# Kernel optimization log

Hardware: AMD Instinct MI355X
Metric: run time of the kernel (lower is better)

The kernel has to match this reference:

```python
import jax, jax.numpy as jnp
import numpy as np

N, E, F, H, S, L, B = 20000, 320000, 64, 256, 32, 128, 16
TAU = 1.0
EPS = 1e-9


def _glorot(k, i, o):
    return (jax.random.normal(k, (i, o), jnp.float32) / np.sqrt(i)).astype(jnp.float32)


def _mlp3(h, w1, b1, w2, b2, w3, b3):
    h = jax.nn.relu(h @ w1 + b1)
    h = jax.nn.relu(h @ w2 + b2)
    return h @ w3 + b3


def _gnn_layer(x, src, dst, w1, b1, w2, b2, w3, b3):
    # PyG: x_i = x[dst] (target), x_j = x[src] (source); aggregate 'add' at target
    m = _mlp3(jnp.concatenate([x[dst], x[src]], axis=1), w1, b1, w2, b2, w3, b3)  # [E, H]
    return jax.ops.segment_sum(m, dst, num_segments=N)  # [N, H]


def _layer_norm(x, g, b):
    mu = x.mean(-1, keepdims=True)
    var = ((x - mu) ** 2).mean(-1, keepdims=True)
    return (x - mu) * jax.lax.rsqrt(var + 1e-5) * g + b


def setup_inputs() -> dict:
    key = jax.random.key(0)
    ks = jax.random.split(key, 32)
    d = {
        'x': jax.random.normal(ks[0], (N, F), jnp.float32),
        'u': jax.random.uniform(ks[1], (N, S), jnp.float32, minval=1e-6, maxval=1.0 - 1e-6),
        'edge_index': jax.random.randint(ks[2], (2, E), 0, N, jnp.int32),
        'batch': jnp.sort(jax.random.randint(ks[3], (N,), 0, B, jnp.int32)),
        # gnn1 MLP: 2F -> H -> H -> H
        'g1w1': _glorot(ks[4], 2 * F, H), 'g1b1': jnp.zeros((H,), jnp.float32),
        'g1w2': _glorot(ks[5], H, H),     'g1b2': jnp.zeros((H,), jnp.float32),
        'g1w3': _glorot(ks[6], H, H),     'g1b3': jnp.zeros((H,), jnp.float32),
        'ln1g': jnp.ones((H,), jnp.float32), 'ln1b': jnp.zeros((H,), jnp.float32),
        # gnn2 MLP: 2H -> H -> H -> H
        'g2w1': _glorot(ks[7], 2 * H, H), 'g2b1': jnp.zeros((H,), jnp.float32),
        'g2w2': _glorot(ks[8], H, H),     'g2b2': jnp.zeros((H,), jnp.float32),
        'g2w3': _glorot(ks[9], H, H),     'g2b3': jnp.zeros((H,), jnp.float32),
        'ln2g': jnp.ones((H,), jnp.float32), 'ln2b': jnp.zeros((H,), jnp.float32),
        # assignment MLP: H -> H -> S
        'aw1': _glorot(ks[10], H, H), 'ab1': jnp.zeros((H,), jnp.float32),
        'aw2': _glorot(ks[11], H, S), 'ab2': jnp.zeros((S,), jnp.float32),
        # output MLP: H -> H -> L
        'ow1': _glorot(ks[12], H, H), 'ob1': jnp.zeros((H,), jnp.float32),
        'ow2': _glorot(ks[13], H, L), 'ob2': jnp.zeros((L,), jnp.float32),
    }
    return d


def reference(x, u, edge_index, batch,
              g1w1, g1b1, g1w2, g1b2, g1w3, g1b3, ln1g, ln1b,
              g2w1, g2b1, g2w2, g2b2, g2w3, g2b3, ln2g, ln2b,
              aw1, ab1, aw2, ab2, ow1, ob1, ow2, ob2):
    src, dst = edge_index[0], edge_index[1]
    x = _layer_norm(jax.nn.relu(_gnn_layer(x, src, dst, g1w1, g1b1, g1w2, g1b2, g1w3, g1b3)), ln1g, ln1b)
    x = _layer_norm(jax.nn.relu(_gnn_layer(x, src, dst, g2w1, g2b1, g2w2, g2b2, g2w3, g2b3)), ln2g, ln2b)
    # Hierarchical pooling with Gumbel-softmax (soft, tau=1.0); u is the uniform noise
    logits = jax.nn.relu(x @ aw1 + ab1) @ aw2 + ab2  # [N, S]
    g = -jnp.log(-jnp.log(u + EPS) + EPS)
    s = jax.nn.softmax((logits + g) / TAU, axis=-1)  # [N, S]
    entropy = -jnp.mean(jnp.sum(s * jnp.log(s + EPS), axis=1))
    avg_s = s.mean(axis=0)
    diversity = jnp.sum(avg_s * jnp.log(avg_s + EPS))
    assign_loss = entropy + diversity
    xe = x[:, None, :] * s[:, :, None]  # [N, S, H]
    pooled = jax.ops.segment_sum(xe, batch, num_segments=B)  # [B, S, H]
    latent = jax.nn.relu(pooled @ ow1 + ob1) @ ow2 + ob2  # [B, S, L]
    return (latent, s, assign_loss)
```

## Files before the change

kernel.cpp:

```cpp
#include <hip/hip_runtime.h>
#include <stdint.h>

#define NN 20000
#define NE 320000
#define NBATCH 16
#define NTILE 2500

typedef short short8 __attribute__((ext_vector_type(8)));
typedef float f32x4  __attribute__((ext_vector_type(4)));

__device__ __forceinline__ unsigned short f2bf(float f) {
  union { float f; unsigned u; } v; v.f = f;
  unsigned r = v.u + 0x7FFFu + ((v.u >> 16) & 1u);
  return (unsigned short)(r >> 16);
}
__device__ __forceinline__ float bf2f(unsigned short h) {
  union { unsigned u; float f; } v; v.u = ((unsigned)h) << 16;
  return v.f;
}
__device__ __forceinline__ float bf2fs(short h) { return bf2f((unsigned short)h); }

#define HOFF(e, k) (((e) << 8) + (((((k) >> 3) ^ ((e) & 7)) << 3) + ((k) & 7)))

struct TD { const float* s; unsigned short* d; int R, C, r0, ld; };
struct TDs { TD t[13]; };

__global__ void wprep(TDs all, const int* __restrict__ dstI, int* __restrict__ deg) {
  if (blockIdx.y == 13) {
    int stride = gridDim.x * blockDim.x;
    for (int e = blockIdx.x * blockDim.x + threadIdx.x; e < NE; e += stride)
      atomicAdd(&deg[dstI[e]], 1);
    return;
  }
  TD td = all.t[blockIdx.y];
  int stride = gridDim.x * blockDim.x;
  int i0 = blockIdx.x * blockDim.x + threadIdx.x;
  if (td.ld == 0) {
    for (int i = i0; i < td.R; i += stride) td.d[i] = f2bf(td.s[i]);
  } else {
    int total = td.R * td.C;
    for (int i = i0; i < total; i += stride) {
      int c = i / td.R;
      int r = i - c * td.R;
      td.d[i] = f2bf(td.s[(size_t)(td.r0 + r) * td.ld + c]);
    }
  }
}

__global__ void scan_bounds(const int* __restrict__ deg, int* __restrict__ rowstart,
                            int* __restrict__ cursor, const int* __restrict__ batch,
                            int* __restrict__ bstart,
                            const float* __restrict__ g1b1, const float* __restrict__ g2b1,
                            float* __restrict__ b1cat1, float* __restrict__ b1cat2) {
  if (blockIdx.x == 0) {
    __shared__ int part[256];
    int t = threadIdx.x;
    int c0 = t * 80; if (c0 > NN) c0 = NN;
    int c1 = c0 + 80; if (c1 > NN) c1 = NN;
    int s = 0;
    for (int i = c0; i < c1; ++i) s += deg[i];
    part[t] = s;
    __syncthreads();
    if (t == 0) {
      int run = 0;
      for (int i = 0; i < 256; ++i) { int v = part[i]; part[i] = run; run += v; }
    }
    __syncthreads();
    int run = part[t];
    for (int i = c0; i < c1; ++i) { rowstart[i] = run; cursor[i] = run; run += deg[i]; }
    if (t == 255) rowstart[NN] = run;
  } else if (blockIdx.x == 80) {
    int t = threadIdx.x;
    b1cat1[t] = g1b1[t]; b1cat1[256 + t] = 0.f;
    b1cat2[t] = g2b1[t]; b1cat2[256 + t] = 0.f;
  } else {
    int n = (blockIdx.x - 1) * 256 + threadIdx.x;
    if (n >= NN) return;
    int bn = batch[n];
    if (n == 0) {
      for (int b2 = 0; b2 <= bn; ++b2) bstart[b2] = 0;
    } else {
      int bp = batch[n - 1];
      for (int b2 = bp + 1; b2 <= bn; ++b2) bstart[b2] = n;
    }
    if (n == NN - 1) {
      for (int b2 = bn + 1; b2 <= NBATCH; ++b2) bstart[b2] = NN;
    }
  }
}

__global__ void fillcsr(const int* __restrict__ srcI, const int* __restrict__ dstI,
                        int* __restrict__ cursor, int* __restrict__ sSrc,
                        int* __restrict__ sDst) {
  int e = blockIdx.x * 256 + threadIdx.x;
  if (e < NE) {
    int d = dstI[e];
    int slot = atomicAdd(&cursor[d], 1);
    sDst[slot] = d;
    sSrc[slot] = srcI[e];
  }
}

__global__ __launch_bounds__(512, 4) void gemmT(
    const unsigned short* __restrict__ WT, const unsigned short* __restrict__ In,
    const float* __restrict__ bias, unsigned short* __restrict__ Out,
    int M, int K, int Nout, int ldo) {
  const int tid = threadIdx.x;
  const int lane = tid & 63, w = tid >> 6;
  const int wf = w >> 1, we = w & 1;
  const int l15 = lane & 15, q = lane >> 4;
  const int fb = blockIdx.x * 256 + wf * 64;
  const int rb = blockIdx.y * 128 + we * 64;
  f32x4 acc[4][4] = {};
  const short8 zz = {0, 0, 0, 0, 0, 0, 0, 0};
  for (int kc = 0; kc < K; kc += 32) {
    short8 a[4], bq[4];
#pragma unroll
    for (int i = 0; i < 4; ++i) {
      if (fb + i * 16 < Nout)
        a[i] = *(const short8*)(WT + (size_t)(fb + i * 16 + l15) * K + kc + q * 8);
      else
        a[i] = zz;
      int r = rb + i * 16 + l15;
      if (r >= M) r = M - 1;
      bq[i] = *(const short8*)(In + (size_t)r * K + kc + q * 8);
    }
#pragma unroll
    for (int i = 0; i < 4; ++i)
#pragma unroll
      for (int j = 0; j < 4; ++j)
        acc[i][j] = __builtin_amdgcn_mfma_f32_16x16x32_bf16(a[i], bq[j], acc[i][j], 0, 0, 0);
  }
#pragma unroll
  for (int i = 0; i < 4; ++i) {
    int f0 = fb + i * 16 + q * 4;
    if (f0 >= Nout) continue;
    float4 bs = make_float4(0.f, 0.f, 0.f, 0.f);
    if (bias) bs = *(const float4*)(bias + f0);
#pragma unroll
    for (int j = 0; j < 4; ++j) {
      int r = rb + j * 16 + l15;
      if (r >= M) continue;
      ushort4 o;
      o.x = f2bf(acc[i][j][0] + bs.x);
      o.y = f2bf(acc[i][j][1] + bs.y);
      o.z = f2bf(acc[i][j][2] + bs.z);
      o.w = f2bf(acc[i][j][3] + bs.w);
      *(ushort4*)(Out + (size_t)r * ldo + f0) = o;
    }
  }
}

__global__ __launch_bounds__(512, 4) void edge_h2agg(
    const unsigned short* __restrict__ PQ, const int* __restrict__ sSrc,
    const int* __restrict__ sDst,
    const unsigned short* __restrict__ W2T, const float* __restrict__ b2,
    int* __restrict__ segcnt, int* __restrict__ segbuf, float* __restrict__ agg) {
  __shared__ __align__(16) unsigned short h[128 * 256];
  const int tid = threadIdx.x;
  const int e0 = blockIdx.x * 128;

  {
    int r = tid & 127;
    int c0 = (tid >> 7) * 64;
    int dn = sDst[e0 + r];
    int sn = sSrc[e0 + r];
    const unsigned short* pd = PQ + (size_t)dn * 512 + c0;
    const unsigned short* ps = PQ + (size_t)sn * 512 + 256 + c0;
#pragma unroll
    for (int i = 0; i < 8; ++i) {
      short8 dv = *(const short8*)(pd + i * 8);
      short8 sv = *(const short8*)(ps + i * 8);
      short8 o;
#pragma unroll
      for (int j = 0; j < 8; ++j) {
        float v = bf2fs(dv[j]) + bf2fs(sv[j]);
        o[j] = (short)f2bf(fmaxf(v, 0.f));
      }
      *(short8*)&h[HOFF(r, c0 + i * 8)] = o;
    }
  }
  __syncthreads();

  const int lane = tid & 63, w = tid >> 6;
  const int wf = w >> 1, we = w & 1;
  const int l15 = lane & 15, q = lane >> 4;
  const int fb = wf * 64, eb = we * 64;
  f32x4 acc[4][4];

#pragma unroll
  for (int i = 0; i < 4; ++i)
#pragma unroll
    for (int j = 0; j < 4; ++j) { f32x4 z = {0.f, 0.f, 0.f, 0.f}; acc[i][j] = z; }
  for (int kc = 0; kc < 256; kc += 32) {
    short8 a[4], bq[4];
#pragma unroll
    for (int i = 0; i < 4; ++i)
      a[i] = *(const short8*)(W2T + (size_t)(fb + i * 16 + l15) * 256 + kc + q * 8);
#pragma unroll
    for (int j = 0; j < 4; ++j)
      bq[j] = *(const short8*)&h[HOFF(eb + j * 16 + l15, kc + q * 8)];
#pragma unroll
    for (int i = 0; i < 4; ++i)
#pragma unroll
      for (int j = 0; j < 4; ++j)
        acc[i][j] = __builtin_amdgcn_mfma_f32_16x16x32_bf16(a[i], bq[j], acc[i][j], 0, 0, 0);
  }
  __syncthreads();
#pragma unroll
  for (int i = 0; i < 4; ++i) {
    int f0 = fb + i * 16 + q * 4;
    float4 bs = *(const float4*)(b2 + f0);
#pragma unroll
    for (int j = 0; j < 4; ++j) {
      int e = eb + j * 16 + l15;
      ushort4 o;
      o.x = f2bf(fmaxf(acc[i][j][0] + bs.x, 0.f));
      o.y = f2bf(fmaxf(acc[i][j][1] + bs.y, 0.f));
      o.z = f2bf(fmaxf(acc[i][j][2] + bs.z, 0.f));
      o.w = f2bf(fmaxf(acc[i][j][3] + bs.w, 0.f));
      *(ushort4*)&h[HOFF(e, f0)] = o;
    }
  }
  if (tid < 128) {
    int d0 = sDst[e0 + tid];
    bool flag = (tid == 0) || (sDst[e0 + tid - 1] != d0);
    if (flag) {
      int idx = atomicAdd(&segcnt[blockIdx.x], 1);
      segbuf[blockIdx.x * 128 + idx] = tid;
    }
  }
  __syncthreads();

  {
    int cnt = segcnt[blockIdx.x];
    int f4 = (tid & 63) * 4;
    int sg = tid >> 6;
    const int* sb = segbuf + blockIdx.x * 128;
    for (int k = sg; k < cnt; k += 8) {
      int start = sb[k];
      int end = 128;
      for (int j2 = 0; j2 < cnt; ++j2) {
        int v = sb[j2];
        if (v > start && v < end) end = v;
      }
      int node = sDst[e0 + start];
      float s0 = 0.f, s1 = 0.f, s2 = 0.f, s3 = 0.f;
      for (int rr = start; rr < end; ++rr) {
        ushort4 v = *(const ushort4*)&h[HOFF(rr, f4)];
        s0 += bf2f(v.x); s1 += bf2f(v.y); s2 += bf2f(v.z); s3 += bf2f(v.w);
      }
      float* pr = agg + (size_t)node * 256 + f4;
      if (start == 0 || end == 128) {
        atomicAdd(pr + 0, s0); atomicAdd(pr + 1, s1);
        atomicAdd(pr + 2, s2); atomicAdd(pr + 3, s3);
      } else {
        *(float4*)pr = make_float4(s0, s1, s2, s3);
      }
    }
  }
}

__global__ __launch_bounds__(512, 4) void node_gemm(
    const unsigned short* __restrict__ W3T, const float* __restrict__ aggH2,
    const float* __restrict__ b3, const int* __restrict__ deg,
    float* __restrict__ outm) {
  const int tid = threadIdx.x;
  const int lane = tid & 63, w = tid >> 6;
  const int wf = w >> 1, we = w & 1;
  const int l15 = lane & 15, q = lane >> 4;
  const int fb = wf * 64;
  const int rb = blockIdx.x * 128 + we * 64;
  f32x4 acc[4][4] = {};
  for (int kc = 0; kc < 256; kc += 32) {
    short8 a[4], bq[4];
#pragma unroll
    for (int i = 0; i < 4; ++i)
      a[i] = *(const short8*)(W3T + (size_t)(fb + i * 16 + l15) * 256 + kc + q * 8);
#pragma unroll
    for (int j = 0; j < 4; ++j) {
      int r = rb + j * 16 + l15;
      if (r >= NN) r = NN - 1;
      const float* pr = aggH2 + (size_t)r * 256 + kc + q * 8;
      float4 lo = *(const float4*)pr;
      float4 hi = *(const float4*)(pr + 4);
      short8 o;
      o[0] = (short)f2bf(lo.x); o[1] = (short)f2bf(lo.y);
      o[2] = (short)f2bf(lo.z); o[3] = (short)f2bf(lo.w);
      o[4] = (short)f2bf(hi.x); o[5] = (short)f2bf(hi.y);
      o[6] = (short)f2bf(hi.z); o[7] = (short)f2bf(hi.w);
      bq[j] = o;
    }
#pragma unroll
    for (int i = 0; i < 4; ++i)
#pragma unroll
      for (int j = 0; j < 4; ++j)
        acc[i][j] = __builtin_amdgcn_mfma_f32_16x16x32_bf16(a[i], bq[j], acc[i][j], 0, 0, 0);
  }
#pragma unroll
  for (int i = 0; i < 4; ++i) {
    int f0 = fb + i * 16 + q * 4;
    float4 b3v = *(const float4*)(b3 + f0);
#pragma unroll
    for (int j = 0; j < 4; ++j) {
      int r = rb + j * 16 + l15;
      if (r >= NN) continue;
      float dg = (float)deg[r];
      *(float4*)(outm + (size_t)r * 256 + f0) =
          make_float4(acc[i][j][0] + dg * b3v.x, acc[i][j][1] + dg * b3v.y,
                      acc[i][j][2] + dg * b3v.z, acc[i][j][3] + dg * b3v.w);
    }
  }
}

__global__ void relu_ln(const float* __restrict__ agg, const float* __restrict__ g,
                        const float* __restrict__ b, unsigned short* __restrict__ out) {
  int row = blockIdx.x * 4 + (threadIdx.x >> 6);
  int lane = threadIdx.x & 63;
  if (row >= NN) return;
  float4 v = *(const float4*)(agg + (size_t)row * 256 + lane * 4);
  v.x = fmaxf(v.x, 0.f); v.y = fmaxf(v.y, 0.f); v.z = fmaxf(v.z, 0.f); v.w = fmaxf(v.w, 0.f);
  float s = v.x + v.y + v.z + v.w;
  float sq = v.x * v.x + v.y * v.y + v.z * v.z + v.w * v.w;
  for (int off = 32; off >= 1; off >>= 1) {
    s += __shfl_xor(s, off);
    sq += __shfl_xor(sq, off);
  }
  float mu = s * (1.f / 256.f);
  float var = sq * (1.f / 256.f) - mu * mu;
  float rs = rsqrtf(var + 1e-5f);
  float4 gg = *(const float4*)(g + lane * 4);
  float4 bb = *(const float4*)(b + lane * 4);
  ushort4 o;
  o.x = f2bf((v.x - mu) * rs * gg.x + bb.x);
  o.y = f2bf((v.y - mu) * rs * gg.y + bb.y);
  o.z = f2bf((v.z - mu) * rs * gg.z + bb.z);
  o.w = f2bf((v.w - mu) * rs * gg.w + bb.w);
  *(ushort4*)(out + (size_t)row * 256 + lane * 4) = o;
}

__global__ __launch_bounds__(512, 4) void assign_gumbel(
    const unsigned short* __restrict__ x2b, const unsigned short* __restrict__ aw1T,
    const float* __restrict__ ab1, const unsigned short* __restrict__ aw2T,
    const float* __restrict__ ab2, const float* __restrict__ u,
    float* __restrict__ sf, float* __restrict__ entacc, float* __restrict__ avgacc) {
  __shared__ __align__(16) unsigned short sh[64 * 256];
  __shared__ float sh_logit[64 * 33];
  __shared__ float lavg[32];
  __shared__ float lent;
  const int tid = threadIdx.x;
  const int n0 = blockIdx.x * 64;
  if (tid < 32) lavg[tid] = 0.f;
  if (tid == 0) lent = 0.f;

  const int lane = tid & 63, w = tid >> 6;
  const int l15 = lane & 15, q = lane >> 4;

  {
    const int wf = w >> 1, we = w & 1;
    const int fb = wf * 64, eb = we * 32;
    f32x4 acc[4][2];
#pragma unroll
    for (int i = 0; i < 4; ++i)
#pragma unroll
      for (int j = 0; j < 2; ++j) { f32x4 z = {0.f, 0.f, 0.f, 0.f}; acc[i][j] = z; }
    for (int kc = 0; kc < 256; kc += 32) {
      short8 a[4], bq[2];
#pragma unroll
      for (int i = 0; i < 4; ++i)
        a[i] = *(const short8*)(aw1T + (size_t)(fb + i * 16 + l15) * 256 + kc + q * 8);
#pragma unroll
      for (int j = 0; j < 2; ++j) {
        int rr = n0 + eb + j * 16 + l15;
        if (rr >= NN) rr = NN - 1;
        bq[j] = *(const short8*)(x2b + (size_t)rr * 256 + kc + q * 8);
      }
#pragma unroll
      for (int i = 0; i < 4; ++i)
#pragma unroll
        for (int j = 0; j < 2; ++j)
          acc[i][j] = __builtin_amdgcn_mfma_f32_16x16x32_bf16(a[i], bq[j], acc[i][j], 0, 0, 0);
    }
#pragma unroll
    for (int i = 0; i < 4; ++i) {
      int f0 = fb + i * 16 + q * 4;
      float4 bs = *(const float4*)(ab1 + f0);
#pragma unroll
      for (int j = 0; j < 2; ++j) {
        int e = eb + j * 16 + l15;
        ushort4 o;
        o.x = f2bf(fmaxf(acc[i][j][0] + bs.x, 0.f));
        o.y = f2bf(fmaxf(acc[i][j][1] + bs.y, 0.f));
        o.z = f2bf(fmaxf(acc[i][j][2] + bs.z, 0.f));
        o.w = f2bf(fmaxf(acc[i][j][3] + bs.w, 0.f));
        *(ushort4*)&sh[HOFF(e, f0)] = o;
      }
    }
  }
  __syncthreads();

  {
    const int rg = w & 3, fg = w >> 2;
    if (fg < 2) {
      f32x4 acc = {0.f, 0.f, 0.f, 0.f};
      for (int kc = 0; kc < 256; kc += 32) {
        short8 a = *(const short8*)(aw2T + (size_t)(fg * 16 + l15) * 256 + kc + q * 8);
        short8 bq = *(const short8*)&sh[HOFF(rg * 16 + l15, kc + q * 8)];
        acc = __builtin_amdgcn_mfma_f32_16x16x32_bf16(a, bq, acc, 0, 0, 0);
      }
      int rowL = rg * 16 + l15;
#pragma unroll
      for (int t2 = 0; t2 < 4; ++t2) {
        int f = fg * 16 + q * 4 + t2;
        sh_logit[rowL * 33 + f] = acc[t2] + ab2[f];
      }
    }
  }
  __syncthreads();

  if (tid < 256) {
    int rowL = tid >> 2, sub = tid & 3;
    int n = n0 + rowL;
    if (n < NN) {
      int j0 = sub * 8;
      float z[8];
      float4 u0 = *(const float4*)(u + (size_t)n * 32 + j0);
      float4 u1 = *(const float4*)(u + (size_t)n * 32 + j0 + 4);
      float uu[8] = {u0.x, u0.y, u0.z, u0.w, u1.x, u1.y, u1.z, u1.w};
      float m = -1e30f;
#pragma unroll
      for (int j = 0; j < 8; ++j) {
        z[j] = sh_logit[rowL * 33 + j0 + j] - logf(-logf(uu[j] + 1e-9f) + 1e-9f);
        m = fmaxf(m, z[j]);
      }
      m = fmaxf(m, __shfl_xor(m, 1));
      m = fmaxf(m, __shfl_xor(m, 2));
      float sum = 0.f;
#pragma unroll
      for (int j = 0; j < 8; ++j) { z[j] = expf(z[j] - m); sum += z[j]; }
      sum += __shfl_xor(sum, 1);
      sum += __shfl_xor(sum, 2);
      float inv = 1.f / sum;
      float ent = 0.f;
      float so[8];
#pragma unroll
      for (int j = 0; j < 8; ++j) {
        float sj = z[j] * inv;
        so[j] = sj;
        ent += sj * logf(sj + 1e-9f);
        atomicAdd(&lavg[j0 + j], sj);
      }
      *(float4*)(sf + (size_t)n * 32 + j0) = make_float4(so[0], so[1], so[2], so[3]);
      *(float4*)(sf + (size_t)n * 32 + j0 + 4) = make_float4(so[4], so[5], so[6], so[7]);
      ent += __shfl_xor(ent, 1);
      ent += __shfl_xor(ent, 2);
      if (sub == 0) atomicAdd(&lent, ent);
    }
  }
  __syncthreads();
  if (tid < 32) atomicAdd(&avgacc[tid], lavg[tid]);
  if (tid == 0) atomicAdd(entacc, lent);
}

__global__ __launch_bounds__(512, 4) void pool_part(
    const unsigned short* __restrict__ x2b, const float* __restrict__ sf,
    const int* __restrict__ bstart, float* __restrict__ part) {
  const int b = blockIdx.x, ci = blockIdx.y;
  const int n0b = bstart[b], n1b = bstart[b + 1];
  const int t = threadIdx.x;
  const int si = t >> 4;
  const int h0 = (t & 15) * 16;
  float acc[16];
#pragma unroll
  for (int k = 0; k < 16; ++k) acc[k] = 0.f;
  for (int nst = n0b + ci * 64; nst < n1b; nst += 16 * 64) {
    int nend = (nst + 64 < n1b) ? nst + 64 : n1b;
    for (int n = nst; n < nend; ++n) {
      float sv = sf[(size_t)n * 32 + si];
      const unsigned short* xr = x2b + (size_t)n * 256 + h0;
      short8 x0 = *(const short8*)xr;
      short8 x1 = *(const short8*)(xr + 8);
#pragma unroll
      for (int j = 0; j < 8; ++j) acc[j] = fmaf(sv, bf2fs(x0[j]), acc[j]);
#pragma unroll
      for (int j = 0; j < 8; ++j) acc[8 + j] = fmaf(sv, bf2fs(x1[j]), acc[8 + j]);
    }
  }
  float* pp = part + (((size_t)b * 16 + ci) << 13) + si * 256 + h0;
#pragma unroll
  for (int k = 0; k < 16; k += 4)
    *(float4*)(pp + k) = make_float4(acc[k], acc[k + 1], acc[k + 2], acc[k + 3]);
}

__global__ void pool_reduce(const float* __restrict__ part, float* __restrict__ pooled) {
  int g = blockIdx.x * 256 + threadIdx.x;
  int b = g >> 13, rem = g & 8191;
  const float* p = part + (((size_t)b * 16) << 13) + rem;
  float s = 0.f;
#pragma unroll
  for (int c = 0; c < 16; ++c) s += p[(size_t)c << 13];
  pooled[g] = s;
}

__global__ __launch_bounds__(512, 4) void out_mlp(
    const float* __restrict__ pooled, const unsigned short* __restrict__ ow1T,
    const float* __restrict__ ob1, const unsigned short* __restrict__ ow2T,
    const float* __restrict__ ob2, float* __restrict__ latent,
    const float* __restrict__ accs, float* __restrict__ outloss) {
  __shared__ __align__(16) unsigned short sh[64 * 256];
  const int tid = threadIdx.x;
  const int n0 = blockIdx.x * 64;
  const int lane = tid & 63, w = tid >> 6;
  const int l15 = lane & 15, q = lane >> 4;

  if (blockIdx.x == 0 && tid < 64) {
    float d = 0.f;
    if (tid < 32) {
      float a = accs[16 + tid] * (1.f / NN);
      d = a * logf(a + 1e-9f);
    }
    for (int off = 32; off >= 1; off >>= 1) d += __shfl_xor(d, off);
    if (tid == 0) outloss[0] = -accs[0] * (1.f / NN) + d;
  }

  {
    const int wf = w >> 1, we = w & 1;
    const int fb = wf * 64, eb = we * 32;
    f32x4 acc[4][2];
#pragma unroll
    for (int i = 0; i < 4; ++i)
#pragma unroll
      for (int j = 0; j < 2; ++j) { f32x4 z = {0.f, 0.f, 0.f, 0.f}; acc[i][j] = z; }
    for (int kc = 0; kc < 256; kc += 32) {
      short8 a[4], bq[2];
#pragma unroll
      for (int i = 0; i < 4; ++i)
        a[i] = *(const short8*)(ow1T + (size_t)(fb + i * 16 + l15) * 256 + kc + q * 8);
#pragma unroll
      for (int j = 0; j < 2; ++j) {
        int rr = n0 + eb + j * 16 + l15;
        const float* pr = pooled + (size_t)rr * 256 + kc + q * 8;
        float4 lo = *(const float4*)pr;
        float4 hi = *(const float4*)(pr + 4);
        short8 o;
        o[0] = (short)f2bf(lo.x); o[1] = (short)f2bf(lo.y);
        o[2] = (short)f2bf(lo.z); o[3] = (short)f2bf(lo.w);
        o[4] = (short)f2bf(hi.x); o[5] = (short)f2bf(hi.y);
        o[6] = (short)f2bf(hi.z); o[7] = (short)f2bf(hi.w);
        bq[j] = o;
      }
#pragma unroll
      for (int i = 0; i < 4; ++i)
#pragma unroll
        for (int j = 0; j < 2; ++j)
          acc[i][j] = __builtin_amdgcn_mfma_f32_16x16x32_bf16(a[i], bq[j], acc[i][j], 0, 0, 0);
    }
#pragma unroll
    for (int i = 0; i < 4; ++i) {
      int f0 = fb + i * 16 + q * 4;
      float4 bs = *(const float4*)(ob1 + f0);
#pragma unroll
      for (int j = 0; j < 2; ++j) {
        int e = eb + j * 16 + l15;
        ushort4 o;
        o.x = f2bf(fmaxf(acc[i][j][0] + bs.x, 0.f));
        o.y = f2bf(fmaxf(acc[i][j][1] + bs.y, 0.f));
        o.z = f2bf(fmaxf(acc[i][j][2] + bs.z, 0.f));
        o.w = f2bf(fmaxf(acc[i][j][3] + bs.w, 0.f));
        *(ushort4*)&sh[HOFF(e, f0)] = o;
      }
    }
  }
  __syncthreads();

  {
    const int wf = w >> 1, we = w & 1;
    const int fb = wf * 32, eb = we * 32;
    f32x4 acc[2][2];
#pragma unroll
    for (int i = 0; i < 2; ++i)
#pragma unroll
      for (int j = 0; j < 2; ++j) { f32x4 z = {0.f, 0.f, 0.f, 0.f}; acc[i][j] = z; }
    for (int kc = 0; kc < 256; kc += 32) {
      short8 a[2], bq[2];
#pragma unroll
      for (int i = 0; i < 2; ++i)
        a[i] = *(const short8*)(ow2T + (size_t)(fb + i * 16 + l15) * 256 + kc + q * 8);
#pragma unroll
      for (int j = 0; j < 2; ++j)
        bq[j] = *(const short8*)&sh[HOFF(eb + j * 16 + l15, kc + q * 8)];
#pragma unroll
      for (int i = 0; i < 2; ++i)
#pragma unroll
        for (int j = 0; j < 2; ++j)
          acc[i][j] = __builtin_amdgcn_mfma_f32_16x16x32_bf16(a[i], bq[j], acc[i][j], 0, 0, 0);
    }
#pragma unroll
    for (int i = 0; i < 2; ++i) {
      int f0 = fb + i * 16 + q * 4;
      float4 bs = *(const float4*)(ob2 + f0);
#pragma unroll
      for (int j = 0; j < 2; ++j) {
        int rr = n0 + eb + j * 16 + l15;
        *(float4*)(latent + (size_t)rr * 128 + f0) =
            make_float4(acc[i][j][0] + bs.x, acc[i][j][1] + bs.y,
                        acc[i][j][2] + bs.z, acc[i][j][3] + bs.w);
      }
    }
  }
}

extern "C" void kernel_launch(void* const* d_in, const int* in_sizes, int n_in,
                              void* d_out, int out_size, void* d_ws, size_t ws_size,
                              hipStream_t stream) {
  (void)in_sizes; (void)n_in; (void)out_size; (void)ws_size;
  const float* x = (const float*)d_in[0];
  const float* u = (const float*)d_in[1];
  const int* ei = (const int*)d_in[2];
  const int* batch = (const int*)d_in[3];
  const float* g1w1 = (const float*)d_in[4];
  const float* g1b1 = (const float*)d_in[5];
  const float* g1w2 = (const float*)d_in[6];
  const float* g1b2 = (const float*)d_in[7];
  const float* g1w3 = (const float*)d_in[8];
  const float* g1b3 = (const float*)d_in[9];
  const float* ln1g = (const float*)d_in[10];
  const float* ln1b = (const float*)d_in[11];
  const float* g2w1 = (const float*)d_in[12];
  const float* g2b1 = (const float*)d_in[13];
  const float* g2w2 = (const float*)d_in[14];
  const float* g2b2 = (const float*)d_in[15];
  const float* g2w3 = (const float*)d_in[16];
  const float* g2b3 = (const float*)d_in[17];
  const float* ln2g = (const float*)d_in[18];
  const float* ln2b = (const float*)d_in[19];
  const float* aw1 = (const float*)d_in[20];
  const float* ab1 = (const float*)d_in[21];
  const float* aw2 = (const float*)d_in[22];
  const float* ab2 = (const float*)d_in[23];
  const float* ow1 = (const float*)d_in[24];
  const float* ob1 = (const float*)d_in[25];
  const float* ow2 = (const float*)d_in[26];
  const float* ob2 = (const float*)d_in[27];
  const int* srcI = ei;
  const int* dstI = ei + NE;

  char* wp = (char*)d_ws;
  size_t off = 0;
  auto alloc = [&](size_t bytes) {
    void* p = wp + off;
    off += (bytes + 255) & ~(size_t)255;
    return p;
  };
  unsigned short* W1catT = (unsigned short*)alloc((size_t)512 * 64 * 2);
  unsigned short* W2catT = (unsigned short*)alloc((size_t)512 * 256 * 2);
  unsigned short* g1w2T = (unsigned short*)alloc((size_t)256 * 256 * 2);
  unsigned short* g1w3T = (unsigned short*)alloc((size_t)256 * 256 * 2);
  unsigned short* g2w2T = (unsigned short*)alloc((size_t)256 * 256 * 2);
  unsigned short* g2w3T = (unsigned short*)alloc((size_t)256 * 256 * 2);
  unsigned short* aw1T = (unsigned short*)alloc((size_t)256 * 256 * 2);
  unsigned short* aw2T = (unsigned short*)alloc((size_t)32 * 256 * 2);
  unsigned short* ow1T = (unsigned short*)alloc((size_t)256 * 256 * 2);
  unsigned short* ow2T = (unsigned short*)alloc((size_t)128 * 256 * 2);
  unsigned short* xb = (unsigned short*)alloc((size_t)NN * 64 * 2);
  unsigned short* PQ = (unsigned short*)alloc((size_t)NN * 512 * 2);
  unsigned short* x1b = (unsigned short*)alloc((size_t)NN * 256 * 2);
  unsigned short* x2b = (unsigned short*)alloc((size_t)NN * 256 * 2);
  int* bstart = (int*)alloc(32 * 4);
  int* cursor = (int*)alloc((size_t)NN * 4);
  int* rowstart = (int*)alloc((size_t)(NN + 1) * 4);
  int* sSrc = (int*)alloc((size_t)NE * 4);
  int* sDst = (int*)alloc((size_t)NE * 4);
  int* segbuf = (int*)alloc((size_t)2 * NTILE * 128 * 4);
  float* b1cat1 = (float*)alloc(512 * 4);
  float* b1cat2 = (float*)alloc(512 * 4);
  char* zbase = (char*)(wp + off);
  float* accs = (float*)alloc(64 * 4);
  float* pooled = (float*)alloc((size_t)512 * 256 * 4);
  int* deg = (int*)alloc((size_t)NN * 4);
  int* segcnt = (int*)alloc((size_t)2 * NTILE * 4);
  float* agg1 = (float*)alloc((size_t)NN * 256 * 4);
  float* agg2 = (float*)alloc((size_t)NN * 256 * 4);
  size_t zbytes = (size_t)((char*)(wp + off) - zbase);

  float* aggm = (float*)PQ;
  float* poolpart = agg1;

  float* out_f = (float*)d_out;
  float* out_latent = out_f;
  float* out_s = out_f + 65536;
  float* out_loss = out_f + 65536 + 640000;

  TDs tds;
  tds.t[0] = {g1w1, W1catT, 64, 256, 0, 256};
  tds.t[1] = {g1w1, W1catT + 256 * 64, 64, 256, 64, 256};
  tds.t[2] = {g1w2, g1w2T, 256, 256, 0, 256};
  tds.t[3] = {g1w3, g1w3T, 256, 256, 0, 256};
  tds.t[4] = {g2w1, W2catT, 256, 256, 0, 256};
  tds.t[5] = {g2w1, W2catT + 256 * 256, 256, 256, 256, 256};
  tds.t[6] = {g2w2, g2w2T, 256, 256, 0, 256};
  tds.t[7] = {g2w3, g2w3T, 256, 256, 0, 256};
  tds.t[8] = {aw1, aw1T, 256, 256, 0, 256};
  tds.t[9] = {aw2, aw2T, 256, 32, 0, 32};
  tds.t[10] = {ow1, ow1T, 256, 256, 0, 256};
  tds.t[11] = {ow2, ow2T, 256, 128, 0, 128};
  tds.t[12] = {x, xb, NN * 64, 1, 0, 0};

  (void)hipMemsetAsync(zbase, 0, zbytes, stream);
  wprep<<<dim3(128, 14), 256, 0, stream>>>(tds, dstI, deg);

  scan_bounds<<<dim3(81), 256, 0, stream>>>(deg, rowstart, cursor, batch, bstart,
                                            g1b1, g2b1, b1cat1, b1cat2);
  fillcsr<<<dim3(1250), 256, 0, stream>>>(srcI, dstI, cursor, sSrc, sDst);

  gemmT<<<dim3(2, 157), 512, 0, stream>>>(W1catT, xb, b1cat1, PQ, NN, 64, 512, 512);
  edge_h2agg<<<dim3(NTILE), 512, 0, stream>>>(PQ, sSrc, sDst, g1w2T, g1b2,
                                              segcnt, segbuf, agg1);
  node_gemm<<<dim3(157), 512, 0, stream>>>(g1w3T, agg1, g1b3, deg, aggm);
  relu_ln<<<dim3(5000), 256, 0, stream>>>(aggm, ln1g, ln1b, x1b);

  gemmT<<<dim3(2, 157), 512, 0, stream>>>(W2catT, x1b, b1cat2, PQ, NN, 256, 512, 512);
  edge_h2agg<<<dim3(NTILE), 512, 0, stream>>>(PQ, sSrc, sDst, g2w2T, g2b2,
                                              segcnt + NTILE, segbuf + (size_t)NTILE * 128, agg2);
  node_gemm<<<dim3(157), 512, 0, stream>>>(g2w3T, agg2, g2b3, deg, aggm);
  relu_ln<<<dim3(5000), 256, 0, stream>>>(aggm, ln2g, ln2b, x2b);

  assign_gumbel<<<dim3(313), 512, 0, stream>>>(x2b, aw1T, ab1, aw2T, ab2, u,
                                               out_s, accs, accs + 16);

  pool_part<<<dim3(16, 16), 512, 0, stream>>>(x2b, out_s, bstart, poolpart);
  pool_reduce<<<dim3(512), 256, 0, stream>>>(poolpart, pooled);

  out_mlp<<<dim3(8), 512, 0, stream>>>(pooled, ow1T, ob1, ow2T, ob2, out_latent,
                                       accs, out_loss);
}
```

Measured before the change: 721.0 us.

## Halve edge tile to 64 edges and use packed bf16 conversion

The edge MLP/aggregation kernel now handles 64 edges per block instead of 128. This halves the LDS footprint and the accumulator registers, so launch bounds can request 6 blocks per CU instead of 4. Float-to-bf16 conversion now uses the hardware v_cvt_pk_bf16_f32 instruction in place of the manual rounding code. The trade-off is twice as many blocks. Each block reloads the W2 weight tile for only half as many edges, and tile boundaries split more segments, so more global atomics are needed.

Result: slower. 841.1 us (+16.7%).

```diff
diff --git a/kernel.cpp b/kernel.cpp
--- a/kernel.cpp
+++ b/kernel.cpp
@@ -4,7 +4,7 @@
 #define NN 20000
 #define NE 320000
 #define NBATCH 16
-#define NTILE 2500
+#define NTILE 5000
 
 typedef short short8 __attribute__((ext_vector_type(8)));
 typedef float f32x4  __attribute__((ext_vector_type(4)));
@@ -19,6 +19,12 @@
   return v.f;
 }
 __device__ __forceinline__ float bf2fs(short h) { return bf2f((unsigned short)h); }
+
+__device__ __forceinline__ unsigned cvt_pk_bf16(float lo, float hi) {
+  unsigned r;
+  asm("v_cvt_pk_bf16_f32 %0, %1, %2" : "=v"(r) : "v"(lo), "v"(hi));
+  return r;
+}
 
 #define HOFF(e, k) (((e) << 8) + (((((k) >> 3) ^ ((e) & 7)) << 3) + ((k) & 7)))
 
@@ -151,33 +157,42 @@
   }
 }
 
-__global__ __launch_bounds__(512, 4) void edge_h2agg(
+__global__ __launch_bounds__(512, 6) void edge_h2agg(
     const unsigned short* __restrict__ PQ, const int* __restrict__ sSrc,
     const int* __restrict__ sDst,
     const unsigned short* __restrict__ W2T, const float* __restrict__ b2,
     int* __restrict__ segcnt, int* __restrict__ segbuf, float* __restrict__ agg) {
-  __shared__ __align__(16) unsigned short h[128 * 256];
+  __shared__ __align__(16) unsigned short h[64 * 256];
   const int tid = threadIdx.x;
-  const int e0 = blockIdx.x * 128;
+  const int e0 = blockIdx.x * 64;
 
   {
-    int r = tid & 127;
-    int c0 = (tid >> 7) * 64;
+    int r = tid & 63;
+    int c0 = (tid >> 6) * 32;
     int dn = sDst[e0 + r];
     int sn = sSrc[e0 + r];
     const unsigned short* pd = PQ + (size_t)dn * 512 + c0;
     const unsigned short* ps = PQ + (size_t)sn * 512 + 256 + c0;
 #pragma unroll
-    for (int i = 0; i < 8; ++i) {
+    for (int i = 0; i < 4; ++i) {
       short8 dv = *(const short8*)(pd + i * 8);
       short8 sv = *(const short8*)(ps + i * 8);
-      short8 o;
-#pragma unroll
-      for (int j = 0; j < 8; ++j) {
-        float v = bf2fs(dv[j]) + bf2fs(sv[j]);
-        o[j] = (short)f2bf(fmaxf(v, 0.f));
-      }
-      *(short8*)&h[HOFF(r, c0 + i * 8)] = o;
+      unsigned pk0, pk1, pk2, pk3;
+      {
+        float a0 = fmaxf(bf2fs(dv[0]) + bf2fs(sv[0]), 0.f);
+        float a1 = fmaxf(bf2fs(dv[1]) + bf2fs(sv[1]), 0.f);
+        pk0 = cvt_pk_bf16(a0, a1);
+        float a2 = fmaxf(bf2fs(dv[2]) + bf2fs(sv[2]), 0.f);
+        float a3 = fmaxf(bf2fs(dv[3]) + bf2fs(sv[3]), 0.f);
+        pk1 = cvt_pk_bf16(a2, a3);
+        float a4 = fmaxf(bf2fs(dv[4]) + bf2fs(sv[4]), 0.f);
+        float a5 = fmaxf(bf2fs(dv[5]) + bf2fs(sv[5]), 0.f);
+        pk2 = cvt_pk_bf16(a4, a5);
+        float a6 = fmaxf(bf2fs(dv[6]) + bf2fs(sv[6]), 0.f);
+        float a7 = fmaxf(bf2fs(dv[7]) + bf2fs(sv[7]), 0.f);
+        pk3 = cvt_pk_bf16(a6, a7);
+      }
+      *(uint4*)&h[HOFF(r, c0 + i * 8)] = make_uint4(pk0, pk1, pk2, pk3);
     }
   }
   __syncthreads();
@@ -185,25 +200,25 @@
   const int lane = tid & 63, w = tid >> 6;
   const int wf = w >> 1, we = w & 1;
   const int l15 = lane & 15, q = lane >> 4;
-  const int fb = wf * 64, eb = we * 64;
-  f32x4 acc[4][4];
+  const int fb = wf * 64, eb = we * 32;
+  f32x4 acc[4][2];
 
 #pragma unroll
   for (int i = 0; i < 4; ++i)
 #pragma unroll
-    for (int j = 0; j < 4; ++j) { f32x4 z = {0.f, 0.f, 0.f, 0.f}; acc[i][j] = z; }
+    for (int j = 0; j < 2; ++j) { f32x4 z = {0.f, 0.f, 0.f, 0.f}; acc[i][j] = z; }
   for (int kc = 0; kc < 256; kc += 32) {
-    short8 a[4], bq[4];
+    short8 a[4], bq[2];
 #pragma unroll
     for (int i = 0; i < 4; ++i)
       a[i] = *(const short8*)(W2T + (size_t)(fb + i * 16 + l15) * 256 + kc + q * 8);
 #pragma unroll
-    for (int j = 0; j < 4; ++j)
+    for (int j = 0; j < 2; ++j)
       bq[j] = *(const short8*)&h[HOFF(eb + j * 16 + l15, kc + q * 8)];
 #pragma unroll
     for (int i = 0; i < 4; ++i)
 #pragma unroll
-      for (int j = 0; j < 4; ++j)
+      for (int j = 0; j < 2; ++j)
         acc[i][j] = __builtin_amdgcn_mfma_f32_16x16x32_bf16(a[i], bq[j], acc[i][j], 0, 0, 0);
   }
   __syncthreads();
@@ -212,22 +227,22 @@
     int f0 = fb + i * 16 + q * 4;
     float4 bs = *(const float4*)(b2 + f0);
 #pragma unroll
-    for (int j = 0; j < 4; ++j) {
+    for (int j = 0; j < 2; ++j) {
       int e = eb + j * 16 + l15;
-      ushort4 o;
-      o.x = f2bf(fmaxf(acc[i][j][0] + bs.x, 0.f));
-      o.y = f2bf(fmaxf(acc[i][j][1] + bs.y, 0.f));
-      o.z = f2bf(fmaxf(acc[i][j][2] + bs.z, 0.f));
-      o.w = f2bf(fmaxf(acc[i][j][3] + bs.w, 0.f));
-      *(ushort4*)&h[HOFF(e, f0)] = o;
-    }
-  }
-  if (tid < 128) {
+      float v0 = fmaxf(acc[i][j][0] + bs.x, 0.f);
+      float v1 = fmaxf(acc[i][j][1] + bs.y, 0.f);
+      float v2 = fmaxf(acc[i][j][2] + bs.z, 0.f);
+      float v3 = fmaxf(acc[i][j][3] + bs.w, 0.f);
+      uint2 o = make_uint2(cvt_pk_bf16(v0, v1), cvt_pk_bf16(v2, v3));
+      *(uint2*)&h[HOFF(e, f0)] = o;
+    }
+  }
+  if (tid < 64) {
     int d0 = sDst[e0 + tid];
     bool flag = (tid == 0) || (sDst[e0 + tid - 1] != d0);
     if (flag) {
       int idx = atomicAdd(&segcnt[blockIdx.x], 1);
-      segbuf[blockIdx.x * 128 + idx] = tid;
+      segbuf[blockIdx.x * 64 + idx] = tid;
     }
   }
   __syncthreads();
@@ -236,10 +251,10 @@
     int cnt = segcnt[blockIdx.x];
     int f4 = (tid & 63) * 4;
     int sg = tid >> 6;
-    const int* sb = segbuf + blockIdx.x * 128;
+    const int* sb = segbuf + blockIdx.x * 64;
     for (int k = sg; k < cnt; k += 8) {
       int start = sb[k];
-      int end = 128;
+      int end = 64;
       for (int j2 = 0; j2 < cnt; ++j2) {
         int v = sb[j2];
         if (v > start && v < end) end = v;
@@ -251,7 +266,7 @@
         s0 += bf2f(v.x); s1 += bf2f(v.y); s2 += bf2f(v.z); s3 += bf2f(v.w);
       }
       float* pr = agg + (size_t)node * 256 + f4;
-      if (start == 0 || end == 128) {
+      if (start == 0 || end == 64) {
         atomicAdd(pr + 0, s0); atomicAdd(pr + 1, s1);
         atomicAdd(pr + 2, s2); atomicAdd(pr + 3, s3);
       } else {
@@ -671,7 +686,7 @@
   int* rowstart = (int*)alloc((size_t)(NN + 1) * 4);
   int* sSrc = (int*)alloc((size_t)NE * 4);
   int* sDst = (int*)alloc((size_t)NE * 4);
-  int* segbuf = (int*)alloc((size_t)2 * NTILE * 128 * 4);
+  int* segbuf = (int*)alloc((size_t)2 * NTILE * 64 * 4);
   float* b1cat1 = (float*)alloc(512 * 4);
   float* b1cat2 = (float*)alloc(512 * 4);
   char* zbase = (char*)(wp + off);
@@ -721,7 +736,7 @@
 
   gemmT<<<dim3(2, 157), 512, 0, stream>>>(W2catT, x1b, b1cat2, PQ, NN, 256, 512, 512);
   edge_h2agg<<<dim3(NTILE), 512, 0, stream>>>(PQ, sSrc, sDst, g2w2T, g2b2,
-                                              segcnt + NTILE, segbuf + (size_t)NTILE * 128, agg2);
+                                              segcnt + NTILE, segbuf + (size_t)NTILE * 64, agg2);
   node_gemm<<<dim3(157), 512, 0, stream>>>(g2w3T, agg2, g2b3, deg, aggm);
   relu_ln<<<dim3(5000), 256, 0, stream>>>(aggm, ln2g, ln2b, x2b);
 
```

## Stage GEMM input rows in swizzled LDS and use packed bf16 conversion

Applied to the files above, without the earlier changes.

The node GEMMs (gemmT, now templated on K, and node_gemm) first load their 128-row input tile into XOR-swizzled shared memory with coalesced vector loads. Previously each wave re-read its rows straight from global memory inside the K loop. node_gemm now converts fp32 to bf16 once while staging, instead of per wave per k-chunk. Scalar round-to-nearest bf16 conversions throughout are replaced with the hardware v_cvt_pk_bf16_f32 instruction. The trade-off is more LDS per block (up to 64 KB), which can limit occupancy, plus an extra barrier.

Result: faster. 679.4 us (-5.8%).

```diff
diff --git a/kernel.cpp b/kernel.cpp
--- a/kernel.cpp
+++ b/kernel.cpp
@@ -20,7 +20,14 @@
 }
 __device__ __forceinline__ float bf2fs(short h) { return bf2f((unsigned short)h); }
 
+__device__ __forceinline__ unsigned cvt_pk_bf16(float lo, float hi) {
+  unsigned r;
+  asm("v_cvt_pk_bf16_f32 %0, %1, %2" : "=v"(r) : "v"(lo), "v"(hi));
+  return r;
+}
+
 #define HOFF(e, k) (((e) << 8) + (((((k) >> 3) ^ ((e) & 7)) << 3) + ((k) & 7)))
+#define HK(e, k, KT) ((e) * (KT) + (((((k) >> 3) ^ ((e) & 7)) << 3) + ((k) & 7)))
 
 struct TD { const float* s; unsigned short* d; int R, C, r0, ld; };
 struct TDs { TD t[13]; };
@@ -101,29 +108,43 @@
   }
 }
 
-__global__ __launch_bounds__(512, 4) void gemmT(
+template <int KT>
+__global__ __launch_bounds__(512, 4) void gemmTs(
     const unsigned short* __restrict__ WT, const unsigned short* __restrict__ In,
     const float* __restrict__ bias, unsigned short* __restrict__ Out,
-    int M, int K, int Nout, int ldo) {
+    int M, int Nout, int ldo) {
+  __shared__ __align__(16) unsigned short h[128 * KT];
   const int tid = threadIdx.x;
+  const int rb0 = blockIdx.y * 128;
+  {
+    int r = tid & 127;
+    int rg = rb0 + r; if (rg >= M) rg = M - 1;
+    const unsigned short* src = In + (size_t)rg * KT + (tid >> 7) * (KT / 4);
+    int c0 = (tid >> 7) * (KT / 4);
+#pragma unroll
+    for (int i = 0; i < KT / 32; ++i) {
+      short8 v = *(const short8*)(src + i * 8);
+      *(short8*)&h[HK(r, c0 + i * 8, KT)] = v;
+    }
+  }
+  __syncthreads();
+
   const int lane = tid & 63, w = tid >> 6;
   const int wf = w >> 1, we = w & 1;
   const int l15 = lane & 15, q = lane >> 4;
   const int fb = blockIdx.x * 256 + wf * 64;
-  const int rb = blockIdx.y * 128 + we * 64;
+  const int rb = rb0 + we * 64;
   f32x4 acc[4][4] = {};
   const short8 zz = {0, 0, 0, 0, 0, 0, 0, 0};
-  for (int kc = 0; kc < K; kc += 32) {
+  for (int kc = 0; kc < KT; kc += 32) {
     short8 a[4], bq[4];
 #pragma unroll
     for (int i = 0; i < 4; ++i) {
       if (fb + i * 16 < Nout)
-        a[i] = *(const short8*)(WT + (size_t)(fb + i * 16 + l15) * K + kc + q * 8);
+        a[i] = *(const short8*)(WT + (size_t)(fb + i * 16 + l15) * KT + kc + q * 8);
       else
         a[i] = zz;
-      int r = rb + i * 16 + l15;
-      if (r >= M) r = M - 1;
-      bq[i] = *(const short8*)(In + (size_t)r * K + kc + q * 8);
+      bq[i] = *(const short8*)&h[HK(we * 64 + i * 16 + l15, kc + q * 8, KT)];
     }
 #pragma unroll
     for (int i = 0; i < 4; ++i)
@@ -141,12 +162,9 @@
     for (int j = 0; j < 4; ++j) {
       int r = rb + j * 16 + l15;
       if (r >= M) continue;
-      ushort4 o;
-      o.x = f2bf(acc[i][j][0] + bs.x);
-      o.y = f2bf(acc[i][j][1] + bs.y);
-      o.z = f2bf(acc[i][j][2] + bs.z);
-      o.w = f2bf(acc[i][j][3] + bs.w);
-      *(ushort4*)(Out + (size_t)r * ldo + f0) = o;
+      uint2 o = make_uint2(cvt_pk_bf16(acc[i][j][0] + bs.x, acc[i][j][1] + bs.y),
+                           cvt_pk_bf16(acc[i][j][2] + bs.z, acc[i][j][3] + bs.w));
+      *(uint2*)(Out + (size_t)r * ldo + f0) = o;
     }
   }
 }
@@ -171,13 +189,17 @@
     for (int i = 0; i < 8; ++i) {
       short8 dv = *(const short8*)(pd + i * 8);
       short8 sv = *(const short8*)(ps + i * 8);
-      short8 o;
-#pragma unroll
-      for (int j = 0; j < 8; ++j) {
-        float v = bf2fs(dv[j]) + bf2fs(sv[j]);
-        o[j] = (short)f2bf(fmaxf(v, 0.f));
-      }
-      *(short8*)&h[HOFF(r, c0 + i * 8)] = o;
+      float a0 = fmaxf(bf2fs(dv[0]) + bf2fs(sv[0]), 0.f);
+      float a1 = fmaxf(bf2fs(dv[1]) + bf2fs(sv[1]), 0.f);
+      float a2 = fmaxf(bf2fs(dv[2]) + bf2fs(sv[2]), 0.f);
+      float a3 = fmaxf(bf2fs(dv[3]) + bf2fs(sv[3]), 0.f);
+      float a4 = fmaxf(bf2fs(dv[4]) + bf2fs(sv[4]), 0.f);
+      float a5 = fmaxf(bf2fs(dv[5]) + bf2fs(sv[5]), 0.f);
+      float a6 = fmaxf(bf2fs(dv[6]) + bf2fs(sv[6]), 0.f);
+      float a7 = fmaxf(bf2fs(dv[7]) + bf2fs(sv[7]), 0.f);
+      uint4 o = make_uint4(cvt_pk_bf16(a0, a1), cvt_pk_bf16(a2, a3),
+                           cvt_pk_bf16(a4, a5), cvt_pk_bf16(a6, a7));
+      *(uint4*)&h[HOFF(r, c0 + i * 8)] = o;
     }
   }
   __syncthreads();
@@ -214,12 +236,12 @@
 #pragma unroll
     for (int j = 0; j < 4; ++j) {
       int e = eb + j * 16 + l15;
-      ushort4 o;
-      o.x = f2bf(fmaxf(acc[i][j][0] + bs.x, 0.f));
-      o.y = f2bf(fmaxf(acc[i][j][1] + bs.y, 0.f));
-      o.z = f2bf(fmaxf(acc[i][j][2] + bs.z, 0.f));
-      o.w = f2bf(fmaxf(acc[i][j][3] + bs.w, 0.f));
-      *(ushort4*)&h[HOFF(e, f0)] = o;
+      float v0 = fmaxf(acc[i][j][0] + bs.x, 0.f);
+      float v1 = fmaxf(acc[i][j][1] + bs.y, 0.f);
+      float v2 = fmaxf(acc[i][j][2] + bs.z, 0.f);
+      float v3 = fmaxf(acc[i][j][3] + bs.w, 0.f);
+      uint2 o = make_uint2(cvt_pk_bf16(v0, v1), cvt_pk_bf16(v2, v3));
+      *(uint2*)&h[HOFF(e, f0)] = o;
     }
   }
   if (tid < 128) {
@@ -265,31 +287,37 @@
     const unsigned short* __restrict__ W3T, const float* __restrict__ aggH2,
     const float* __restrict__ b3, const int* __restrict__ deg,
     float* __restrict__ outm) {
+  __shared__ __align__(16) unsigned short h[128 * 256];
   const int tid = threadIdx.x;
+  const int rb0 = blockIdx.x * 128;
+  {
+    int r = tid & 127;
+    int rg = rb0 + r; if (rg >= NN) rg = NN - 1;
+    int c0 = (tid >> 7) * 64;
+    const float* src = aggH2 + (size_t)rg * 256 + c0;
+#pragma unroll
+    for (int i = 0; i < 8; ++i) {
+      float4 lo = *(const float4*)(src + i * 8);
+      float4 hi = *(const float4*)(src + i * 8 + 4);
+      uint4 o = make_uint4(cvt_pk_bf16(lo.x, lo.y), cvt_pk_bf16(lo.z, lo.w),
+                           cvt_pk_bf16(hi.x, hi.y), cvt_pk_bf16(hi.z, hi.w));
+      *(uint4*)&h[HOFF(r, c0 + i * 8)] = o;
+    }
+  }
+  __syncthreads();
+
   const int lane = tid & 63, w = tid >> 6;
   const int wf = w >> 1, we = w & 1;
   const int l15 = lane & 15, q = lane >> 4;
   const int fb = wf * 64;
-  const int rb = blockIdx.x * 128 + we * 64;
+  const int rb = rb0 + we * 64;
   f32x4 acc[4][4] = {};
   for (int kc = 0; kc < 256; kc += 32) {
     short8 a[4], bq[4];
 #pragma unroll
-    for (int i = 0; i < 4; ++i)
+    for (int i = 0; i < 4; ++i) {
       a[i] = *(const short8*)(W3T + (size_t)(fb + i * 16 + l15) * 256 + kc + q * 8);
-#pragma unroll
-    for (int j = 0; j < 4; ++j) {
-      int r = rb + j * 16 + l15;
-      if (r >= NN) r = NN - 1;
-      const float* pr = aggH2 + (size_t)r * 256 + kc + q * 8;
-      float4 lo = *(const float4*)pr;
-      float4 hi = *(const float4*)(pr + 4);
-      short8 o;
-      o[0] = (short)f2bf(lo.x); o[1] = (short)f2bf(lo.y);
-      o[2] = (short)f2bf(lo.z); o[3] = (short)f2bf(lo.w);
-      o[4] = (short)f2bf(hi.x); o[5] = (short)f2bf(hi.y);
-      o[6] = (short)f2bf(hi.z); o[7] = (short)f2bf(hi.w);
-      bq[j] = o;
+      bq[i] = *(const short8*)&h[HOFF(we * 64 + i * 16 + l15, kc + q * 8)];
     }
 #pragma unroll
     for (int i = 0; i < 4; ++i)
@@ -713,13 +741,13 @@
                                             g1b1, g2b1, b1cat1, b1cat2);
   fillcsr<<<dim3(1250), 256, 0, stream>>>(srcI, dstI, cursor, sSrc, sDst);
 
-  gemmT<<<dim3(2, 157), 512, 0, stream>>>(W1catT, xb, b1cat1, PQ, NN, 64, 512, 512);
+  gemmTs<64><<<dim3(2, 157), 512, 0, stream>>>(W1catT, xb, b1cat1, PQ, NN, 512, 512);
   edge_h2agg<<<dim3(NTILE), 512, 0, stream>>>(PQ, sSrc, sDst, g1w2T, g1b2,
                                               segcnt, segbuf, agg1);
   node_gemm<<<dim3(157), 512, 0, stream>>>(g1w3T, agg1, g1b3, deg, aggm);
   relu_ln<<<dim3(5000), 256, 0, stream>>>(aggm, ln1g, ln1b, x1b);
 
-  gemmT<<<dim3(2, 157), 512, 0, stream>>>(W2catT, x1b, b1cat2, PQ, NN, 256, 512, 512);
+  gemmTs<256><<<dim3(2, 157), 512, 0, stream>>>(W2catT, x1b, b1cat2, PQ, NN, 512, 512);
   edge_h2agg<<<dim3(NTILE), 512, 0, stream>>>(PQ, sSrc, sDst, g2w2T, g2b2,
                                               segcnt + NTILE, segbuf + (size_t)NTILE * 128, agg2);
   node_gemm<<<dim3(157), 512, 0, stream>>>(g2w3T, agg2, g2b3, deg, aggm);
```
